# Performance work log

Hardware: AMD Instinct MI355X
Metric: run time of the kernel (lower is better)

The kernel has to match this reference:

```python
import jax, jax.numpy as jnp
import numpy as np

B, T, E, H = 2, 2048, 1024, 16
D = E // H  # head_dim = 64


def setup_inputs() -> dict:
    key = jax.random.key(0)
    kx, kq, kk, kv, ko = jax.random.split(key, 5)
    x = jax.random.normal(kx, (B, T, E), dtype=jnp.float32)
    # nn.Parameter(torch.randn(...)) -> standard normal params
    Wq = jax.random.normal(kq, (H, E, D), dtype=jnp.float32)
    Wk = jax.random.normal(kk, (H, E, D), dtype=jnp.float32)
    Wv = jax.random.normal(kv, (H, E, D), dtype=jnp.float32)
    # nn.Linear(E, E, bias=False): weight [out, in], y = a @ Wo.T
    Wo = jax.random.normal(ko, (E, E), dtype=jnp.float32) * (1.0 / np.sqrt(E))
    # boolean mask: True positions are filled with -inf (causal: strict upper tri)
    mask = jnp.triu(jnp.ones((T, T), dtype=bool), k=1)
    return {"x": x, "mask": mask, "Wq": Wq, "Wk": Wk, "Wv": Wv, "Wo": Wo}


def reference(x, mask, Wq, Wk, Wv, Wo):
    # x: [b, t, e]; Wq/Wk/Wv: [h, e, i]
    q = jnp.einsum('hei,bte->hbti', Wq, x)
    k = jnp.einsum('hei,bte->hbti', Wk, x)
    v = jnp.einsum('hei,bte->hbti', Wv, x)
    # NOTE: original scales by sqrt(seq_len) (x.shape[1]), not sqrt(head_dim)
    scale = x.shape[1] ** 0.5
    fit = jnp.einsum('hbti,hbTi->hbtT', q, k) / scale  # [h, b, t, T]
    fit = jnp.where(mask, -jnp.inf, fit)
    p = jax.nn.softmax(fit, axis=-1)
    att = jnp.einsum('hbtT,hbTi->hbti', p, v)          # [h, b, t, i]
    # rearrange 'h b t i -> b t (h i)'
    b, t = att.shape[1], att.shape[2]
    att = jnp.transpose(att, (1, 2, 0, 3)).reshape(b, t, -1)
    return att @ Wo.T
```

## Files before the change

kernel.cpp:

```cpp
#include <hip/hip_runtime.h>
#include <hip/hip_fp8.h>
#include <stdint.h>

constexpr float INV_SCALE = 0.022097086912079608f;
constexpr float LOG2E = 1.4426950408889634f;
constexpr float QSC = INV_SCALE * LOG2E;

typedef __attribute__((ext_vector_type(8))) short bfrag;
typedef __attribute__((ext_vector_type(4))) float facc;
typedef __attribute__((ext_vector_type(4))) unsigned short us4;

#define MFMA(a, b, c) __builtin_amdgcn_mfma_f32_16x16x32_bf16((a), (b), (c), 0, 0, 0)
#define EXP2(x) __builtin_amdgcn_exp2f(x)

__device__ __forceinline__ unsigned short f2bh(float f) {
    union { float f; unsigned int u; } cv; cv.f = f;
    unsigned int u = cv.u;
    u += 0x7FFFu + ((u >> 16) & 1u);
    return (unsigned short)(u >> 16);
}
__device__ __forceinline__ float bh2f(unsigned short h) {
    union { unsigned int u; float f; } cv; cv.u = ((unsigned int)h) << 16;
    return cv.f;
}
__device__ __forceinline__ void gl_lds16(const unsigned short* g, unsigned short* lds) {
    __builtin_amdgcn_global_load_lds(
        (const __attribute__((address_space(1))) unsigned int*)g,
        (__attribute__((address_space(3))) unsigned int*)lds, 16, 0, 0);
}
__device__ __forceinline__ bfrag f8frag(uint2 raw) {
    union { uint2 u; unsigned char b[8]; } cv; cv.u = raw;
    bfrag r;
    #pragma unroll
    for (int j = 0; j < 8; ++j) {
        const __hip_fp8_e4m3* t = reinterpret_cast<const __hip_fp8_e4m3*>(&cv.b[j]);
        r[j] = (short)f2bh((float)(*t) * 0.00390625f);
    }
    return r;
}
template<int CTRL>
__device__ __forceinline__ float dppmax(float v) {
    int s = __builtin_amdgcn_update_dpp(0, __builtin_bit_cast(int, v), CTRL, 0xF, 0xF, true);
    return fmaxf(v, __builtin_bit_cast(float, s));
}
__device__ __forceinline__ float rowmax16(float v) {
    v = dppmax<0xB1>(v);
    v = dppmax<0x4E>(v);
    v = dppmax<0x141>(v);
    v = dppmax<0x140>(v);
    return v;
}

__global__ __launch_bounds__(256) void prep_xw(const float* __restrict__ x,
                                               const float* __restrict__ Wo,
                                               unsigned short* __restrict__ xh,
                                               unsigned short* __restrict__ xl,
                                               unsigned short* __restrict__ WoB) {
    if (blockIdx.x < 1024) {
        int idx = blockIdx.x * 256 + threadIdx.x;
        facc v = *(const facc*)&Wo[(size_t)idx * 4];
        us4 o;
        #pragma unroll
        for (int j = 0; j < 4; ++j) o[j] = f2bh(v[j]);
        *(us4*)&WoB[(size_t)idx * 4] = o;
    } else {
        int idx = (blockIdx.x - 1024) * 256 + threadIdx.x;
        facc v = *(const facc*)&x[(size_t)idx * 4];
        us4 hv, lv;
        #pragma unroll
        for (int j = 0; j < 4; ++j) {
            unsigned short hb = f2bh(v[j]);
            hv[j] = hb;
            lv[j] = f2bh(v[j] - bh2f(hb));
        }
        *(us4*)&xh[(size_t)idx * 4] = hv;
        *(us4*)&xl[(size_t)idx * 4] = lv;
    }
}

__global__ __launch_bounds__(256) void prep_w(
    const float* __restrict__ Wq, const float* __restrict__ Wk, const float* __restrict__ Wv,
    unsigned short* __restrict__ WqTh, unsigned short* __restrict__ WqTl,
    unsigned short* __restrict__ WkTh, unsigned short* __restrict__ WkTl,
    unsigned short* __restrict__ WvT)
{
    __shared__ float tile[64][65];
    const int tid = threadIdx.x;
    const int et = blockIdx.x, h = blockIdx.y, m = blockIdx.z;
    const float* W = (m == 0) ? Wq : (m == 1) ? Wk : Wv;
    #pragma unroll
    for (int rep = 0; rep < 4; ++rep) {
        int idx = rep * 256 + tid;
        int e = idx >> 4, i4 = (idx & 15) * 4;
        facc v = *(const facc*)&W[(size_t)h * 65536 + (size_t)(et * 64 + e) * 64 + i4];
        tile[e][i4] = v.x; tile[e][i4 + 1] = v.y; tile[e][i4 + 2] = v.z; tile[e][i4 + 3] = v.w;
    }
    __syncthreads();
    unsigned short* Oh = (m == 0) ? WqTh : (m == 1) ? WkTh : WvT;
    unsigned short* Ol = (m == 0) ? WqTl : WkTl;
    #pragma unroll
    for (int rep = 0; rep < 4; ++rep) {
        int idx = rep * 256 + tid;
        int i = idx >> 4, e4 = (idx & 15) * 4;
        us4 hv, lv;
        #pragma unroll
        for (int j = 0; j < 4; ++j) {
            float f = tile[e4 + j][i];
            unsigned short hb = f2bh(f);
            hv[j] = hb;
            lv[j] = f2bh(f - bh2f(hb));
        }
        size_t o = (size_t)(h * 64 + i) * 1024 + et * 64 + e4;
        *(us4*)&Oh[o] = hv;
        if (m < 2) *(us4*)&Ol[o] = lv;
    }
}

__global__ __launch_bounds__(256, 2) void qkv_fused(
    const unsigned short* __restrict__ xh, const unsigned short* __restrict__ xl,
    const unsigned short* __restrict__ WqTh, const unsigned short* __restrict__ WqTl,
    const unsigned short* __restrict__ WkTh, const unsigned short* __restrict__ WkTl,
    const unsigned short* __restrict__ WvT,
    unsigned short* __restrict__ qh, unsigned char* __restrict__ ql8,
    unsigned short* __restrict__ kh, unsigned short* __restrict__ kl,
    unsigned short* __restrict__ vT)
{
    extern __shared__ unsigned short sm[];
    unsigned short* Ab = sm;
    unsigned short* Qb = sm + 16384;
    unsigned short* Kb = sm + 24576;
    unsigned short* Vb = sm + 32768;
    const int tid = threadIdx.x;
    const int w = tid >> 6, l = tid & 63;
    const int wm = w >> 1, wn = w & 1;
    const int ct = blockIdx.x, rt = blockIdx.y;

    const int lc = (l & 7) ^ (l >> 3);
    const int krel = (lc & 3) * 8;
    const unsigned short* Axp = (lc < 4) ? xh : xl;
    const unsigned short* Qp  = (lc < 4) ? WqTh : WqTl;
    const unsigned short* Kp  = (lc < 4) ? WkTh : WkTl;
    const int lcv = (l & 3) ^ ((l >> 3) & 3);

    facc accq[4][2], acck[4][2], accv[4][2];
    #pragma unroll
    for (int m = 0; m < 4; ++m)
        #pragma unroll
        for (int n = 0; n < 2; ++n) {
            accq[m][n] = (facc)(0.0f); acck[m][n] = (facc)(0.0f); accv[m][n] = (facc)(0.0f);
        }

    auto stage = [&](int buf, int e0) {
        #pragma unroll
        for (int i = 0; i < 4; ++i) {
            int slice = w * 4 + i;
            int row = slice * 8 + (l >> 3);
            gl_lds16(&Axp[(size_t)(rt * 128 + row) * 1024 + e0 + krel],
                     &Ab[buf * 8192 + slice * 512]);
        }
        #pragma unroll
        for (int i = 0; i < 2; ++i) {
            int slice = w * 2 + i;
            int row = slice * 8 + (l >> 3);
            size_t sb = (size_t)(ct * 64 + row) * 1024 + e0 + krel;
            gl_lds16(&Qp[sb], &Qb[buf * 4096 + slice * 512]);
            gl_lds16(&Kp[sb], &Kb[buf * 4096 + slice * 512]);
        }
        {
            int row = w * 16 + (l >> 2);
            gl_lds16(&WvT[(size_t)(ct * 64 + row) * 1024 + e0 + lcv * 8],
                     &Vb[w * 1024 + (l & 63) * 0 + w * 0 + (w * 1024) * 0 + w * 1024 - w * 1024 + w * 1024 + 0]);
        }
    };
    auto stageV_fix = [&](int buf, int e0) {
        int row = w * 16 + (l >> 2);
        gl_lds16(&WvT[(size_t)(ct * 64 + row) * 1024 + e0 + lcv * 8],
                 &Vb[buf * 2048 + w * 512]);
    };

    {
        #pragma unroll
        for (int i = 0; i < 4; ++i) {
            int slice = w * 4 + i;
            int row = slice * 8 + (l >> 3);
            gl_lds16(&Axp[(size_t)(rt * 128 + row) * 1024 + krel], &Ab[slice * 512]);
        }
        #pragma unroll
        for (int i = 0; i < 2; ++i) {
            int slice = w * 2 + i;
            int row = slice * 8 + (l >> 3);
            size_t sb = (size_t)(ct * 64 + row) * 1024 + krel;
            gl_lds16(&Qp[sb], &Qb[slice * 512]);
            gl_lds16(&Kp[sb], &Kb[slice * 512]);
        }
        stageV_fix(0, 0);
    }
    asm volatile("s_waitcnt vmcnt(0)" ::: "memory");
    __builtin_amdgcn_s_barrier();

    for (int t = 0; t < 32; ++t) {
        __builtin_amdgcn_s_barrier();
        __builtin_amdgcn_sched_barrier(0);
        if (t < 31) {
            int buf = (t + 1) & 1, e0 = (t + 1) * 32;
            #pragma unroll
            for (int i = 0; i < 4; ++i) {
                int slice = w * 4 + i;
                int row = slice * 8 + (l >> 3);
                gl_lds16(&Axp[(size_t)(rt * 128 + row) * 1024 + e0 + krel],
                         &Ab[buf * 8192 + slice * 512]);
            }
            #pragma unroll
            for (int i = 0; i < 2; ++i) {
                int slice = w * 2 + i;
                int row = slice * 8 + (l >> 3);
                size_t sb = (size_t)(ct * 64 + row) * 1024 + e0 + krel;
                gl_lds16(&Qp[sb], &Qb[buf * 4096 + slice * 512]);
                gl_lds16(&Kp[sb], &Kb[buf * 4096 + slice * 512]);
            }
            stageV_fix(buf, e0);
        }
        __builtin_amdgcn_sched_barrier(0);
        if (t < 31) asm volatile("s_waitcnt vmcnt(9)" ::: "memory");
        else        asm volatile("s_waitcnt vmcnt(0)" ::: "memory");
        __builtin_amdgcn_sched_barrier(0);
        __builtin_amdgcn_s_barrier();
        __builtin_amdgcn_sched_barrier(0);

        const unsigned short* Ac = &Ab[(t & 1) * 8192];
        const unsigned short* Qc = &Qb[(t & 1) * 4096];
        const unsigned short* Kc = &Kb[(t & 1) * 4096];
        const unsigned short* Vc = &Vb[(t & 1) * 2048];
        const int ca = (l >> 4) ^ (l & 7);
        const int cb = ca ^ 4;

        bfrag afh[4], afl[4];
        #pragma unroll
        for (int m = 0; m < 4; ++m) {
            int row = wm * 64 + m * 16 + (l & 15);
            afh[m] = *(const bfrag*)&Ac[row * 64 + ca * 8];
            afl[m] = *(const bfrag*)&Ac[row * 64 + cb * 8];
        }
        #pragma unroll
        for (int n = 0; n < 2; ++n) {
            int nr = wn * 32 + n * 16 + (l & 15);
            int cv = (l >> 4) ^ ((nr >> 1) & 3);
            bfrag bv = *(const bfrag*)&Vc[nr * 32 + cv * 8];
            #pragma unroll
            for (int m = 0; m < 4; ++m) accv[m][n] = MFMA(afh[m], bv, accv[m][n]);
        }
        #pragma unroll
        for (int n = 0; n < 2; ++n) {
            int nr = wn * 32 + n * 16 + (l & 15);
            bfrag bh = *(const bfrag*)&Qc[nr * 64 + ca * 8];
            bfrag bl = *(const bfrag*)&Qc[nr * 64 + cb * 8];
            #pragma unroll
            for (int m = 0; m < 4; ++m) {
                accq[m][n] = MFMA(afh[m], bh, accq[m][n]);
                accq[m][n] = MFMA(afh[m], bl, accq[m][n]);
                accq[m][n] = MFMA(afl[m], bh, accq[m][n]);
            }
        }
        #pragma unroll
        for (int n = 0; n < 2; ++n) {
            int nr = wn * 32 + n * 16 + (l & 15);
            bfrag bh = *(const bfrag*)&Kc[nr * 64 + ca * 8];
            bfrag bl = *(const bfrag*)&Kc[nr * 64 + cb * 8];
            #pragma unroll
            for (int m = 0; m < 4; ++m) {
                acck[m][n] = MFMA(afh[m], bh, acck[m][n]);
                acck[m][n] = MFMA(afh[m], bl, acck[m][n]);
                acck[m][n] = MFMA(afl[m], bh, acck[m][n]);
            }
        }
    }

    #pragma unroll
    for (int m = 0; m < 4; ++m)
        #pragma unroll
        for (int r = 0; r < 4; ++r) {
            int row = rt * 128 + wm * 64 + m * 16 + (l >> 4) * 4 + r;
            #pragma unroll
            for (int n = 0; n < 2; ++n) {
                int col = ct * 64 + wn * 32 + n * 16 + (l & 15);
                float fq = accq[m][n][r] * QSC;
                unsigned short hb = f2bh(fq);
                qh[(size_t)row * 1024 + col] = hb;
                __hip_fp8_e4m3 e((fq - bh2f(hb)) * 256.0f);
                ql8[(size_t)row * 1024 + col] = *reinterpret_cast<unsigned char*>(&e);
                float fk = acck[m][n][r];
                unsigned short kb = f2bh(fk);
                kh[(size_t)row * 1024 + col] = kb;
                kl[(size_t)row * 1024 + col] = f2bh(fk - bh2f(kb));
            }
        }
    #pragma unroll
    for (int m = 0; m < 4; ++m) {
        int t0g = rt * 128 + wm * 64 + m * 16 + (l >> 4) * 4;
        int b_ = t0g >> 11, t0 = t0g & 2047;
        #pragma unroll
        for (int n = 0; n < 2; ++n) {
            int col = ct * 64 + wn * 32 + n * 16 + (l & 15);
            int h_ = col >> 6, d = col & 63;
            us4 pk;
            #pragma unroll
            for (int r = 0; r < 4; ++r) pk[r] = f2bh(accv[m][n][r]);
            *(us4*)&vT[((size_t)((h_ * 2 + b_) * 64 + d)) * 2048 + t0] = pk;
        }
    }
}

__device__ __forceinline__ void stage_kv(
    const unsigned short* __restrict__ kh, const unsigned short* __restrict__ kl,
    const unsigned short* __restrict__ vT,
    unsigned short* Khb, unsigned short* Klb, unsigned short* Vtb,
    int w, int l, int b, int h, int kt)
{
    #pragma unroll
    for (int i = 0; i < 2; ++i) {
        int pbase = (w * 2 + i) * 1024;
        int p = pbase + l * 16;
        int row = p >> 7, slot = (p >> 4) & 7;
        int chunk = slot ^ (row & 7);
        size_t srcK = (size_t)(b * 2048 + kt * 64 + row) * 1024 + h * 64 + chunk * 8;
        size_t srcV = ((size_t)(h * 2 + b) * 64 + row) * 2048 + (size_t)kt * 64 + chunk * 8;
        gl_lds16(&kh[srcK], &Khb[pbase >> 1]);
        gl_lds16(&kl[srcK], &Klb[pbase >> 1]);
        gl_lds16(&vT[srcV], &Vtb[pbase >> 1]);
    }
}

__device__ __forceinline__ void attn_step(
    const unsigned short* Khb, const unsigned short* Klb, const unsigned short* Vtb,
    unsigned short* Pl, const bfrag* qfh, const bfrag* qfl,
    facc* O, facc& Osum, float* mrow, bfrag ones, int w, int l, bool diag)
{
    facc S[4];
    #pragma unroll
    for (int f = 0; f < 4; ++f) S[f] = (facc)(0.0f);
    __builtin_amdgcn_s_setprio(1);
    #pragma unroll
    for (int s = 0; s < 2; ++s) {
        #pragma unroll
        for (int f = 0; f < 4; ++f) {
            int key = f * 16 + (l & 15);
            int ch = (s * 4 + (l >> 4)) ^ (key & 7);
            bfrag kbh = *(const bfrag*)&Khb[key * 64 + ch * 8];
            bfrag kbl = *(const bfrag*)&Klb[key * 64 + ch * 8];
            S[f] = MFMA(qfh[s], kbh, S[f]);
            S[f] = MFMA(qfh[s], kbl, S[f]);
            S[f] = MFMA(qfl[s], kbh, S[f]);
        }
    }
    __builtin_amdgcn_s_setprio(0);
    if (diag) {
        #pragma unroll
        for (int f = 0; f < 4; ++f) {
            int keyl = f * 16 + (l & 15);
            #pragma unroll
            for (int r = 0; r < 4; ++r) {
                int qls = w * 16 + (l >> 4) * 4 + r;
                if (keyl > qls) S[f][r] = -1e30f;
            }
        }
    }
    float mx[4];
    float dmax = -3.0e38f;
    #pragma unroll
    for (int r = 0; r < 4; ++r) {
        float m0 = fmaxf(fmaxf(S[0][r], S[1][r]), fmaxf(S[2][r], S[3][r]));
        m0 = rowmax16(m0);
        mx[r] = m0;
        dmax = fmaxf(dmax, m0 - mrow[r]);
    }
    if (!__all(dmax <= 8.0f)) {
        #pragma unroll
        for (int r = 0; r < 4; ++r) {
            float mn = fmaxf(mrow[r], mx[r]);
            float fac = EXP2(mrow[r] - mn);
            mrow[r] = mn;
            O[0][r] *= fac; O[1][r] *= fac; O[2][r] *= fac; O[3][r] *= fac;
            Osum[r] *= fac;
        }
    }
    #pragma unroll
    for (int r = 0; r < 4; ++r)
        #pragma unroll
        for (int f = 0; f < 4; ++f) S[f][r] = EXP2(S[f][r] - mrow[r]);
    #pragma unroll
    for (int f = 0; f < 4; ++f) {
        int key = f * 16 + (l & 15);
        #pragma unroll
        for (int r = 0; r < 4; ++r) {
            int qr = w * 16 + (l >> 4) * 4 + r;
            Pl[qr * 64 + (((key >> 3) ^ (qr & 7)) * 8) + (key & 7)] = f2bh(S[f][r]);
        }
    }
    __builtin_amdgcn_s_setprio(1);
    #pragma unroll
    for (int s = 0; s < 2; ++s) {
        int qa = w * 16 + (l & 15);
        int cha = (s * 4 + (l >> 4)) ^ (qa & 7);
        bfrag pa = *(const bfrag*)&Pl[qa * 64 + cha * 8];
        Osum = MFMA(pa, ones, Osum);
        #pragma unroll
        for (int f = 0; f < 4; ++f) {
            int d = f * 16 + (l & 15);
            int chv = (s * 4 + (l >> 4)) ^ (d & 7);
            bfrag vb = *(const bfrag*)&Vtb[d * 64 + chv * 8];
            O[f] = MFMA(pa, vb, O[f]);
        }
    }
    __builtin_amdgcn_s_setprio(0);
}

__global__ __launch_bounds__(256, 2) void attn_mfma(
    const unsigned short* __restrict__ qh, const unsigned char* __restrict__ ql8,
    const unsigned short* __restrict__ kh, const unsigned short* __restrict__ kl,
    const unsigned short* __restrict__ vT, unsigned short* __restrict__ att)
{
    __shared__ unsigned short Kh[2][4096], Kl[2][4096], Vt[2][4096], Pl[4096];
    const int tid = threadIdx.x, w = tid >> 6, l = tid & 63;
    const int dd = blockIdx.y * 16 + blockIdx.x;
    const int xcd = dd & 7, sl = dd >> 3;
    const int hb = xcd * 4 + (sl >> 4);
    const int bx = sl & 15;
    const int qtA = 31 - bx, qtB = bx;
    const int h = hb >> 1, b = hb & 1;

    bfrag ones;
    #pragma unroll
    for (int j = 0; j < 8; ++j) ones[j] = (short)0x3F80;

    bfrag qfhA[2], qflA[2], qfhB[2], qflB[2];
    {
        const int qrowA = qtA * 64 + w * 16 + (l & 15);
        const size_t qoffA = (size_t)(b * 2048 + qrowA) * 1024 + h * 64 + (l >> 4) * 8;
        qfhA[0] = *(const bfrag*)&qh[qoffA];
        qfhA[1] = *(const bfrag*)&qh[qoffA + 32];
        qflA[0] = f8frag(*(const uint2*)&ql8[qoffA]);
        qflA[1] = f8frag(*(const uint2*)&ql8[qoffA + 32]);
        const int qrowB = qtB * 64 + w * 16 + (l & 15);
        const size_t qoffB = (size_t)(b * 2048 + qrowB) * 1024 + h * 64 + (l >> 4) * 8;
        qfhB[0] = *(const bfrag*)&qh[qoffB];
        qfhB[1] = *(const bfrag*)&qh[qoffB + 32];
        qflB[0] = f8frag(*(const uint2*)&ql8[qoffB]);
        qflB[1] = f8frag(*(const uint2*)&ql8[qoffB + 32]);
    }

    facc OA[4], OB[4], OsA, OsB;
    float mA[4], mB[4];
    #pragma unroll
    for (int f = 0; f < 4; ++f) { OA[f] = (facc)(0.0f); OB[f] = (facc)(0.0f); }
    OsA = (facc)(0.0f); OsB = (facc)(0.0f);
    #pragma unroll
    for (int r = 0; r < 4; ++r) { mA[r] = -1e30f; mB[r] = -1e30f; }

    stage_kv(kh, kl, vT, Kh[0], Kl[0], Vt[0], w, l, b, h, 0);
    for (int kt = 0; kt <= qtA; ++kt) {
        const int cur = kt & 1;
        __syncthreads();
        if (kt < qtA)
            stage_kv(kh, kl, vT, Kh[cur ^ 1], Kl[cur ^ 1], Vt[cur ^ 1], w, l, b, h, kt + 1);
        __builtin_amdgcn_sched_barrier(0);
        __builtin_amdgcn_s_barrier();
        __builtin_amdgcn_sched_barrier(0);
        attn_step(Kh[cur], Kl[cur], Vt[cur], Pl, qfhA, qflA, OA, OsA, mA, ones,
                  w, l, kt == qtA);
        if (kt <= qtB)
            attn_step(Kh[cur], Kl[cur], Vt[cur], Pl, qfhB, qflB, OB, OsB, mB, ones,
                      w, l, kt == qtB);
    }

    #pragma unroll
    for (int f = 0; f < 4; ++f) {
        int d = h * 64 + f * 16 + (l & 15);
        #pragma unroll
        for (int r = 0; r < 4; ++r) {
            int tA = qtA * 64 + w * 16 + (l >> 4) * 4 + r;
            att[(size_t)(b * 2048 + tA) * 1024 + d] = f2bh(OA[f][r] / OsA[r]);
            int tB = qtB * 64 + w * 16 + (l >> 4) * 4 + r;
            att[(size_t)(b * 2048 + tB) * 1024 + d] = f2bh(OB[f][r] / OsB[r]);
        }
    }
}

__global__ __launch_bounds__(256, 2) void outproj(
    const unsigned short* __restrict__ att, const unsigned short* __restrict__ WoB,
    float* __restrict__ out)
{
    __shared__ unsigned short Ab[2][128 * 64], Bb[2][128 * 64];
    const int tid = threadIdx.x, w = tid >> 6, l = tid & 63;
    const int wm = w >> 1, wn = w & 1;
    const int rt = blockIdx.x, ct = blockIdx.y;

    const int lc = (l & 7) ^ (l >> 3);
    facc acc[4][4];
    #pragma unroll
    for (int i = 0; i < 4; ++i)
        #pragma unroll
        for (int j = 0; j < 4; ++j) acc[i][j] = (facc)(0.0f);

    auto stage = [&](int buf, int e0) {
        #pragma unroll
        for (int i = 0; i < 4; ++i) {
            int slice = w * 4 + i;
            int row = slice * 8 + (l >> 3);
            gl_lds16(&att[(size_t)(rt * 128 + row) * 1024 + e0 + lc * 8], &Ab[buf][slice * 512]);
            gl_lds16(&WoB[(size_t)(ct * 128 + row) * 1024 + e0 + lc * 8], &Bb[buf][slice * 512]);
        }
    };

    stage(0, 0);
    int cur = 0;
    for (int t = 0; t < 16; ++t) {
        __syncthreads();
        if (t < 15) stage(cur ^ 1, (t + 1) * 64);
        __builtin_amdgcn_sched_barrier(0);
        __builtin_amdgcn_s_barrier();
        __builtin_amdgcn_sched_barrier(0);
        #pragma unroll
        for (int s = 0; s < 2; ++s) {
            const int slot = (s * 4 + (l >> 4)) ^ (l & 7);
            bfrag af[4], bf_[4];
            #pragma unroll
            for (int m = 0; m < 4; ++m)
                af[m] = *(const bfrag*)&Ab[cur][(wm * 64 + m * 16 + (l & 15)) * 64 + slot * 8];
            #pragma unroll
            for (int n = 0; n < 4; ++n)
                bf_[n] = *(const bfrag*)&Bb[cur][(wn * 64 + n * 16 + (l & 15)) * 64 + slot * 8];
            #pragma unroll
            for (int m = 0; m < 4; ++m)
                #pragma unroll
                for (int n = 0; n < 4; ++n)
                    acc[m][n] = MFMA(af[m], bf_[n], acc[m][n]);
        }
        cur ^= 1;
    }
    #pragma unroll
    for (int m = 0; m < 4; ++m)
        #pragma unroll
        for (int r = 0; r < 4; ++r) {
            int row = rt * 128 + wm * 64 + m * 16 + (l >> 4) * 4 + r;
            #pragma unroll
            for (int n = 0; n < 4; ++n) {
                int col = ct * 128 + wn * 64 + n * 16 + (l & 15);
                out[(size_t)row * 1024 + col] = acc[m][n][r];
            }
        }
}

extern "C" void kernel_launch(void* const* d_in, const int* in_sizes, int n_in,
                              void* d_out, int out_size, void* d_ws, size_t ws_size,
                              hipStream_t stream) {
    const float* x  = (const float*)d_in[0];
    const float* Wq = (const float*)d_in[2];
    const float* Wk = (const float*)d_in[3];
    const float* Wv = (const float*)d_in[4];
    const float* Wo = (const float*)d_in[5];

    uint8_t* wsb = (uint8_t*)d_ws;
    const size_t MB = 1024 * 1024;
    unsigned short* WqTh = (unsigned short*)(wsb + 0 * MB);
    unsigned short* WqTl = (unsigned short*)(wsb + 2 * MB);
    unsigned short* WkTh = (unsigned short*)(wsb + 4 * MB);
    unsigned short* WkTl = (unsigned short*)(wsb + 6 * MB);
    unsigned short* WvT  = (unsigned short*)(wsb + 8 * MB);
    unsigned short* qh   = (unsigned short*)(wsb + 10 * MB);
    unsigned char*  ql8  = (unsigned char*)(wsb + 18 * MB);
    unsigned short* kh   = (unsigned short*)(wsb + 22 * MB);
    unsigned short* kl   = (unsigned short*)(wsb + 30 * MB);
    unsigned short* vT   = (unsigned short*)(wsb + 38 * MB);
    unsigned short* att  = (unsigned short*)(wsb + 46 * MB);
    unsigned short* xh   = (unsigned short*)(wsb + 46 * MB);
    unsigned short* WoB  = (unsigned short*)(wsb + 54 * MB);
    unsigned short* xl   = (unsigned short*)(wsb + 56 * MB);

    hipFuncSetAttribute((const void*)qkv_fused,
                        hipFuncAttributeMaxDynamicSharedMemorySize, 73728);

    prep_xw<<<dim3(5120), 256, 0, stream>>>(x, Wo, xh, xl, WoB);
    prep_w<<<dim3(16, 16, 3), 256, 0, stream>>>(Wq, Wk, Wv, WqTh, WqTl, WkTh, WkTl, WvT);
    qkv_fused<<<dim3(16, 32), 256, 73728, stream>>>(xh, xl, WqTh, WqTl, WkTh, WkTl, WvT,
                                                    qh, ql8, kh, kl, vT);
    attn_mfma<<<dim3(16, 32), 256, 0, stream>>>(qh, ql8, kh, kl, vT, att);
    outproj<<<dim3(32, 8), 256, 0, stream>>>(att, WoB, (float*)d_out);
}
```

Baseline: 164.5 us.

## Split paired query tiles into separate blocks and single-buffer V staging

The attention kernel used to give each block two query tiles (a long and a short one, for causal load balance). It now launches one block per query tile, 1024 blocks, ordered longest-first. V is single-buffered and loaded during the QK^T/softmax phase, with a wait and barrier placed before the PV matmul. Shared memory use is lower, which allows launch bounds of 3 blocks per SM, trading per-block K reuse across two query tiles for more parallelism and occupancy. V load latency is now only partly hidden, and the extra barrier adds a sync point each iteration.

```diff
diff --git a/kernel.cpp b/kernel.cpp
--- a/kernel.cpp
+++ b/kernel.cpp
@@ -150,29 +150,7 @@
             accq[m][n] = (facc)(0.0f); acck[m][n] = (facc)(0.0f); accv[m][n] = (facc)(0.0f);
         }
 
-    auto stage = [&](int buf, int e0) {
-        #pragma unroll
-        for (int i = 0; i < 4; ++i) {
-            int slice = w * 4 + i;
-            int row = slice * 8 + (l >> 3);
-            gl_lds16(&Axp[(size_t)(rt * 128 + row) * 1024 + e0 + krel],
-                     &Ab[buf * 8192 + slice * 512]);
-        }
-        #pragma unroll
-        for (int i = 0; i < 2; ++i) {
-            int slice = w * 2 + i;
-            int row = slice * 8 + (l >> 3);
-            size_t sb = (size_t)(ct * 64 + row) * 1024 + e0 + krel;
-            gl_lds16(&Qp[sb], &Qb[buf * 4096 + slice * 512]);
-            gl_lds16(&Kp[sb], &Kb[buf * 4096 + slice * 512]);
-        }
-        {
-            int row = w * 16 + (l >> 2);
-            gl_lds16(&WvT[(size_t)(ct * 64 + row) * 1024 + e0 + lcv * 8],
-                     &Vb[w * 1024 + (l & 63) * 0 + w * 0 + (w * 1024) * 0 + w * 1024 - w * 1024 + w * 1024 + 0]);
-        }
-    };
-    auto stageV_fix = [&](int buf, int e0) {
+    auto stageV = [&](int buf, int e0) {
         int row = w * 16 + (l >> 2);
         gl_lds16(&WvT[(size_t)(ct * 64 + row) * 1024 + e0 + lcv * 8],
                  &Vb[buf * 2048 + w * 512]);
@@ -193,7 +171,7 @@
             gl_lds16(&Qp[sb], &Qb[slice * 512]);
             gl_lds16(&Kp[sb], &Kb[slice * 512]);
         }
-        stageV_fix(0, 0);
+        stageV(0, 0);
     }
     asm volatile("s_waitcnt vmcnt(0)" ::: "memory");
     __builtin_amdgcn_s_barrier();
@@ -218,7 +196,7 @@
                 gl_lds16(&Qp[sb], &Qb[buf * 4096 + slice * 512]);
                 gl_lds16(&Kp[sb], &Kb[buf * 4096 + slice * 512]);
             }
-            stageV_fix(buf, e0);
+            stageV(buf, e0);
         }
         __builtin_amdgcn_sched_barrier(0);
         if (t < 31) asm volatile("s_waitcnt vmcnt(9)" ::: "memory");
@@ -310,11 +288,9 @@
     }
 }
 
-__device__ __forceinline__ void stage_kv(
+__device__ __forceinline__ void stage_k(
     const unsigned short* __restrict__ kh, const unsigned short* __restrict__ kl,
-    const unsigned short* __restrict__ vT,
-    unsigned short* Khb, unsigned short* Klb, unsigned short* Vtb,
-    int w, int l, int b, int h, int kt)
+    unsigned short* Khb, unsigned short* Klb, int w, int l, int b, int h, int kt)
 {
     #pragma unroll
     for (int i = 0; i < 2; ++i) {
@@ -323,153 +299,154 @@
         int row = p >> 7, slot = (p >> 4) & 7;
         int chunk = slot ^ (row & 7);
         size_t srcK = (size_t)(b * 2048 + kt * 64 + row) * 1024 + h * 64 + chunk * 8;
-        size_t srcV = ((size_t)(h * 2 + b) * 64 + row) * 2048 + (size_t)kt * 64 + chunk * 8;
         gl_lds16(&kh[srcK], &Khb[pbase >> 1]);
         gl_lds16(&kl[srcK], &Klb[pbase >> 1]);
+    }
+}
+__device__ __forceinline__ void stage_v(
+    const unsigned short* __restrict__ vT, unsigned short* Vtb,
+    int w, int l, int b, int h, int kt)
+{
+    #pragma unroll
+    for (int i = 0; i < 2; ++i) {
+        int pbase = (w * 2 + i) * 1024;
+        int p = pbase + l * 16;
+        int row = p >> 7, slot = (p >> 4) & 7;
+        int chunk = slot ^ (row & 7);
+        size_t srcV = ((size_t)(h * 2 + b) * 64 + row) * 2048 + (size_t)kt * 64 + chunk * 8;
         gl_lds16(&vT[srcV], &Vtb[pbase >> 1]);
     }
 }
 
-__device__ __forceinline__ void attn_step(
-    const unsigned short* Khb, const unsigned short* Klb, const unsigned short* Vtb,
-    unsigned short* Pl, const bfrag* qfh, const bfrag* qfl,
-    facc* O, facc& Osum, float* mrow, bfrag ones, int w, int l, bool diag)
-{
-    facc S[4];
-    #pragma unroll
-    for (int f = 0; f < 4; ++f) S[f] = (facc)(0.0f);
-    __builtin_amdgcn_s_setprio(1);
-    #pragma unroll
-    for (int s = 0; s < 2; ++s) {
-        #pragma unroll
-        for (int f = 0; f < 4; ++f) {
-            int key = f * 16 + (l & 15);
-            int ch = (s * 4 + (l >> 4)) ^ (key & 7);
-            bfrag kbh = *(const bfrag*)&Khb[key * 64 + ch * 8];
-            bfrag kbl = *(const bfrag*)&Klb[key * 64 + ch * 8];
-            S[f] = MFMA(qfh[s], kbh, S[f]);
-            S[f] = MFMA(qfh[s], kbl, S[f]);
-            S[f] = MFMA(qfl[s], kbh, S[f]);
-        }
-    }
-    __builtin_amdgcn_s_setprio(0);
-    if (diag) {
-        #pragma unroll
-        for (int f = 0; f < 4; ++f) {
-            int keyl = f * 16 + (l & 15);
-            #pragma unroll
-            for (int r = 0; r < 4; ++r) {
-                int qls = w * 16 + (l >> 4) * 4 + r;
-                if (keyl > qls) S[f][r] = -1e30f;
-            }
-        }
-    }
-    float mx[4];
-    float dmax = -3.0e38f;
-    #pragma unroll
-    for (int r = 0; r < 4; ++r) {
-        float m0 = fmaxf(fmaxf(S[0][r], S[1][r]), fmaxf(S[2][r], S[3][r]));
-        m0 = rowmax16(m0);
-        mx[r] = m0;
-        dmax = fmaxf(dmax, m0 - mrow[r]);
-    }
-    if (!__all(dmax <= 8.0f)) {
-        #pragma unroll
-        for (int r = 0; r < 4; ++r) {
-            float mn = fmaxf(mrow[r], mx[r]);
-            float fac = EXP2(mrow[r] - mn);
-            mrow[r] = mn;
-            O[0][r] *= fac; O[1][r] *= fac; O[2][r] *= fac; O[3][r] *= fac;
-            Osum[r] *= fac;
-        }
-    }
-    #pragma unroll
-    for (int r = 0; r < 4; ++r)
-        #pragma unroll
-        for (int f = 0; f < 4; ++f) S[f][r] = EXP2(S[f][r] - mrow[r]);
-    #pragma unroll
-    for (int f = 0; f < 4; ++f) {
-        int key = f * 16 + (l & 15);
-        #pragma unroll
-        for (int r = 0; r < 4; ++r) {
-            int qr = w * 16 + (l >> 4) * 4 + r;
-            Pl[qr * 64 + (((key >> 3) ^ (qr & 7)) * 8) + (key & 7)] = f2bh(S[f][r]);
-        }
-    }
-    __builtin_amdgcn_s_setprio(1);
-    #pragma unroll
-    for (int s = 0; s < 2; ++s) {
-        int qa = w * 16 + (l & 15);
-        int cha = (s * 4 + (l >> 4)) ^ (qa & 7);
-        bfrag pa = *(const bfrag*)&Pl[qa * 64 + cha * 8];
-        Osum = MFMA(pa, ones, Osum);
-        #pragma unroll
-        for (int f = 0; f < 4; ++f) {
-            int d = f * 16 + (l & 15);
-            int chv = (s * 4 + (l >> 4)) ^ (d & 7);
-            bfrag vb = *(const bfrag*)&Vtb[d * 64 + chv * 8];
-            O[f] = MFMA(pa, vb, O[f]);
-        }
-    }
-    __builtin_amdgcn_s_setprio(0);
-}
-
-__global__ __launch_bounds__(256, 2) void attn_mfma(
+__global__ __launch_bounds__(256, 3) void attn_mfma(
     const unsigned short* __restrict__ qh, const unsigned char* __restrict__ ql8,
     const unsigned short* __restrict__ kh, const unsigned short* __restrict__ kl,
     const unsigned short* __restrict__ vT, unsigned short* __restrict__ att)
 {
-    __shared__ unsigned short Kh[2][4096], Kl[2][4096], Vt[2][4096], Pl[4096];
+    __shared__ unsigned short Kh[2][4096], Kl[2][4096], Vt[4096], Pl[4096];
     const int tid = threadIdx.x, w = tid >> 6, l = tid & 63;
-    const int dd = blockIdx.y * 16 + blockIdx.x;
+    const int dd = blockIdx.y * 32 + blockIdx.x;
     const int xcd = dd & 7, sl = dd >> 3;
-    const int hb = xcd * 4 + (sl >> 4);
-    const int bx = sl & 15;
-    const int qtA = 31 - bx, qtB = bx;
+    const int qt = 31 - (sl >> 2);
+    const int hb = xcd * 4 + (sl & 3);
     const int h = hb >> 1, b = hb & 1;
 
     bfrag ones;
     #pragma unroll
     for (int j = 0; j < 8; ++j) ones[j] = (short)0x3F80;
 
-    bfrag qfhA[2], qflA[2], qfhB[2], qflB[2];
+    bfrag qfh[2], qfl[2];
     {
-        const int qrowA = qtA * 64 + w * 16 + (l & 15);
-        const size_t qoffA = (size_t)(b * 2048 + qrowA) * 1024 + h * 64 + (l >> 4) * 8;
-        qfhA[0] = *(const bfrag*)&qh[qoffA];
-        qfhA[1] = *(const bfrag*)&qh[qoffA + 32];
-        qflA[0] = f8frag(*(const uint2*)&ql8[qoffA]);
-        qflA[1] = f8frag(*(const uint2*)&ql8[qoffA + 32]);
-        const int qrowB = qtB * 64 + w * 16 + (l & 15);
-        const size_t qoffB = (size_t)(b * 2048 + qrowB) * 1024 + h * 64 + (l >> 4) * 8;
-        qfhB[0] = *(const bfrag*)&qh[qoffB];
-        qfhB[1] = *(const bfrag*)&qh[qoffB + 32];
-        qflB[0] = f8frag(*(const uint2*)&ql8[qoffB]);
-        qflB[1] = f8frag(*(const uint2*)&ql8[qoffB + 32]);
-    }
-
-    facc OA[4], OB[4], OsA, OsB;
-    float mA[4], mB[4];
-    #pragma unroll
-    for (int f = 0; f < 4; ++f) { OA[f] = (facc)(0.0f); OB[f] = (facc)(0.0f); }
-    OsA = (facc)(0.0f); OsB = (facc)(0.0f);
-    #pragma unroll
-    for (int r = 0; r < 4; ++r) { mA[r] = -1e30f; mB[r] = -1e30f; }
-
-    stage_kv(kh, kl, vT, Kh[0], Kl[0], Vt[0], w, l, b, h, 0);
-    for (int kt = 0; kt <= qtA; ++kt) {
+        const int qrow = qt * 64 + w * 16 + (l & 15);
+        const size_t qoff = (size_t)(b * 2048 + qrow) * 1024 + h * 64 + (l >> 4) * 8;
+        qfh[0] = *(const bfrag*)&qh[qoff];
+        qfh[1] = *(const bfrag*)&qh[qoff + 32];
+        qfl[0] = f8frag(*(const uint2*)&ql8[qoff]);
+        qfl[1] = f8frag(*(const uint2*)&ql8[qoff + 32]);
+    }
+
+    facc O[4], Osum;
+    float mrow[4];
+    #pragma unroll
+    for (int f = 0; f < 4; ++f) O[f] = (facc)(0.0f);
+    Osum = (facc)(0.0f);
+    #pragma unroll
+    for (int r = 0; r < 4; ++r) mrow[r] = -1e30f;
+
+    stage_k(kh, kl, Kh[0], Kl[0], w, l, b, h, 0);
+    for (int kt = 0; kt <= qt; ++kt) {
         const int cur = kt & 1;
         __syncthreads();
-        if (kt < qtA)
-            stage_kv(kh, kl, vT, Kh[cur ^ 1], Kl[cur ^ 1], Vt[cur ^ 1], w, l, b, h, kt + 1);
+        stage_v(vT, Vt, w, l, b, h, kt);
+        if (kt < qt)
+            stage_k(kh, kl, Kh[cur ^ 1], Kl[cur ^ 1], w, l, b, h, kt + 1);
         __builtin_amdgcn_sched_barrier(0);
         __builtin_amdgcn_s_barrier();
         __builtin_amdgcn_sched_barrier(0);
-        attn_step(Kh[cur], Kl[cur], Vt[cur], Pl, qfhA, qflA, OA, OsA, mA, ones,
-                  w, l, kt == qtA);
-        if (kt <= qtB)
-            attn_step(Kh[cur], Kl[cur], Vt[cur], Pl, qfhB, qflB, OB, OsB, mB, ones,
-                      w, l, kt == qtB);
+
+        facc S[4];
+        #pragma unroll
+        for (int f = 0; f < 4; ++f) S[f] = (facc)(0.0f);
+        __builtin_amdgcn_s_setprio(1);
+        #pragma unroll
+        for (int s = 0; s < 2; ++s) {
+            #pragma unroll
+            for (int f = 0; f < 4; ++f) {
+                int key = f * 16 + (l & 15);
+                int ch = (s * 4 + (l >> 4)) ^ (key & 7);
+                bfrag kbh = *(const bfrag*)&Kh[cur][key * 64 + ch * 8];
+                bfrag kbl = *(const bfrag*)&Kl[cur][key * 64 + ch * 8];
+                S[f] = MFMA(qfh[s], kbh, S[f]);
+                S[f] = MFMA(qfh[s], kbl, S[f]);
+                S[f] = MFMA(qfl[s], kbh, S[f]);
+            }
+        }
+        __builtin_amdgcn_s_setprio(0);
+        if (kt == qt) {
+            #pragma unroll
+            for (int f = 0; f < 4; ++f) {
+                int keyl = f * 16 + (l & 15);
+                #pragma unroll
+                for (int r = 0; r < 4; ++r) {
+                    int qls = w * 16 + (l >> 4) * 4 + r;
+                    if (keyl > qls) S[f][r] = -1e30f;
+                }
+            }
+        }
+        float mx[4];
+        float dmax = -3.0e38f;
+        #pragma unroll
+        for (int r = 0; r < 4; ++r) {
+            float m0 = fmaxf(fmaxf(S[0][r], S[1][r]), fmaxf(S[2][r], S[3][r]));
+            m0 = rowmax16(m0);
+            mx[r] = m0;
+            dmax = fmaxf(dmax, m0 - mrow[r]);
+        }
+        if (!__all(dmax <= 8.0f)) {
+            #pragma unroll
+            for (int r = 0; r < 4; ++r) {
+                float mn = fmaxf(mrow[r], mx[r]);
+                float fac = EXP2(mrow[r] - mn);
+                mrow[r] = mn;
+                O[0][r] *= fac; O[1][r] *= fac; O[2][r] *= fac; O[3][r] *= fac;
+                Osum[r] *= fac;
+            }
+        }
+        #pragma unroll
+        for (int r = 0; r < 4; ++r)
+            #pragma unroll
+            for (int f = 0; f < 4; ++f) S[f][r] = EXP2(S[f][r] - mrow[r]);
+        #pragma unroll
+        for (int f = 0; f < 4; ++f) {
+            int key = f * 16 + (l & 15);
+            #pragma unroll
+            for (int r = 0; r < 4; ++r) {
+                int qr = w * 16 + (l >> 4) * 4 + r;
+                Pl[qr * 64 + (((key >> 3) ^ (qr & 7)) * 8) + (key & 7)] = f2bh(S[f][r]);
+            }
+        }
+        __builtin_amdgcn_sched_barrier(0);
+        if (kt < qt) asm volatile("s_waitcnt vmcnt(4)" ::: "memory");
+        else         asm volatile("s_waitcnt vmcnt(0)" ::: "memory");
+        __builtin_amdgcn_sched_barrier(0);
+        __builtin_amdgcn_s_barrier();
+        __builtin_amdgcn_sched_barrier(0);
+        __builtin_amdgcn_s_setprio(1);
+        #pragma unroll
+        for (int s = 0; s < 2; ++s) {
+            int qa = w * 16 + (l & 15);
+            int cha = (s * 4 + (l >> 4)) ^ (qa & 7);
+            bfrag pa = *(const bfrag*)&Pl[qa * 64 + cha * 8];
+            Osum = MFMA(pa, ones, Osum);
+            #pragma unroll
+            for (int f = 0; f < 4; ++f) {
+                int d = f * 16 + (l & 15);
+                int chv = (s * 4 + (l >> 4)) ^ (d & 7);
+                bfrag vb = *(const bfrag*)&Vt[d * 64 + chv * 8];
+                O[f] = MFMA(pa, vb, O[f]);
+            }
+        }
+        __builtin_amdgcn_s_setprio(0);
     }
 
     #pragma unroll
@@ -477,10 +454,8 @@
         int d = h * 64 + f * 16 + (l & 15);
         #pragma unroll
         for (int r = 0; r < 4; ++r) {
-            int tA = qtA * 64 + w * 16 + (l >> 4) * 4 + r;
-            att[(size_t)(b * 2048 + tA) * 1024 + d] = f2bh(OA[f][r] / OsA[r]);
-            int tB = qtB * 64 + w * 16 + (l >> 4) * 4 + r;
-            att[(size_t)(b * 2048 + tB) * 1024 + d] = f2bh(OB[f][r] / OsB[r]);
+            int t = qt * 64 + w * 16 + (l >> 4) * 4 + r;
+            att[(size_t)(b * 2048 + t) * 1024 + d] = f2bh(O[f][r] / Osum[r]);
         }
     }
 }
@@ -583,6 +558,6 @@
     prep_w<<<dim3(16, 16, 3), 256, 0, stream>>>(Wq, Wk, Wv, WqTh, WqTl, WkTh, WkTl, WvT);
     qkv_fused<<<dim3(16, 32), 256, 73728, stream>>>(xh, xl, WqTh, WqTl, WkTh, WkTl, WvT,
                                                     qh, ql8, kh, kl, vT);
-    attn_mfma<<<dim3(16, 32), 256, 0, stream>>>(qh, ql8, kh, kl, vT, att);
+    attn_mfma<<<dim3(32, 32), 256, 0, stream>>>(qh, ql8, kh, kl, vT, att);
     outproj<<<dim3(32, 8), 256, 0, stream>>>(att, WoB, (float*)d_out);
 }
```

New measurement: 156.6 us. 1.05x faster.
